# Performance work log

Measured on AMD Instinct MI355X. Metric: run time of the kernel, lower is better.

Reference implementation:

```python
import jax, jax.numpy as jnp
import numpy as np

N_HEADS, D_MODEL, D_HEAD = 16, 1024, 64
INIT_STD = 0.02
IGNORE = -100000.0


def setup_inputs() -> dict:
    key = jax.random.key(0)
    ks = jax.random.split(key, 5)
    x = jax.random.normal(ks[0], (2, 2048, D_MODEL), dtype=jnp.float32)
    W_Q = INIT_STD * jax.random.normal(ks[1], (N_HEADS, D_MODEL, D_HEAD), dtype=jnp.float32)
    W_K = INIT_STD * jax.random.normal(ks[2], (N_HEADS, D_MODEL, D_HEAD), dtype=jnp.float32)
    W_V = INIT_STD * jax.random.normal(ks[3], (N_HEADS, D_MODEL, D_HEAD), dtype=jnp.float32)
    W_O = INIT_STD * jax.random.normal(ks[4], (N_HEADS, D_HEAD, D_MODEL), dtype=jnp.float32)
    b_Q = jnp.zeros((N_HEADS, D_HEAD), dtype=jnp.float32)
    b_K = jnp.zeros((N_HEADS, D_HEAD), dtype=jnp.float32)
    b_V = jnp.zeros((N_HEADS, D_HEAD), dtype=jnp.float32)
    b_O = jnp.zeros((D_MODEL,), dtype=jnp.float32)
    return {"normalized_resid_pre": x, "W_Q": W_Q, "W_K": W_K, "W_V": W_V,
            "W_O": W_O, "b_Q": b_Q, "b_K": b_K, "b_V": b_V, "b_O": b_O}


def reference(normalized_resid_pre, W_Q, W_K, W_V, W_O, b_Q, b_K, b_V, b_O):
    x = normalized_resid_pre  # [b, s, d_model]
    q = jnp.einsum('bsm,hmd->bshd', x, W_Q) + b_Q  # [b, s, h, d_head]
    k = jnp.einsum('bsm,hmd->bshd', x, W_K) + b_K
    v = jnp.einsum('bsm,hmd->bshd', x, W_V) + b_V
    scores = jnp.einsum('bqhd,bkhd->bhqk', q, k) / jnp.sqrt(jnp.float32(D_HEAD))
    s = x.shape[1]
    causal = jnp.triu(jnp.ones((s, s), dtype=bool), k=1)  # True above diagonal
    scores = jnp.where(causal, jnp.float32(IGNORE), scores)
    pattern = jax.nn.softmax(scores, axis=-1)  # [b, h, q, k]
    z = jnp.einsum('bkhd,bhqk->bqhd', v, pattern)
    attn_out = jnp.einsum('bqhd,hdm->bqm', z, W_O) + b_O
    return attn_out
```

## Files before the change

kernel.cpp:

```cpp
#include <hip/hip_runtime.h>
#include <hip/hip_bf16.h>

#define BB   2
#define SS   2048
#define HH   16
#define DM_  1024
#define DH_  64
#define NROW 4096
#define NQKV 3072

typedef unsigned short u16;
typedef unsigned int u32;
using short4v = __attribute__((ext_vector_type(4))) short;
using short8 = __attribute__((ext_vector_type(8))) short;
using bf16x8 = __attribute__((ext_vector_type(8))) __bf16;
using f32x4  = __attribute__((ext_vector_type(4))) float;
using f32x16 = __attribute__((ext_vector_type(16))) float;

#define QSCALE 0.180336880f

__device__ __forceinline__ u16 f2bf(float f) {
    union { float f; unsigned u; } v; v.f = f;
    unsigned r = v.u + 0x7fffu + ((v.u >> 16) & 1u);
    return (u16)(r >> 16);
}

__device__ __forceinline__ f32x4 mfma16(bf16x8 a, bf16x8 b, f32x4 c) {
    return __builtin_amdgcn_mfma_f32_16x16x32_bf16(a, b, c, 0, 0, 0);
}
__device__ __forceinline__ f32x16 mfma32(bf16x8 a, bf16x8 b, f32x16 c) {
    return __builtin_amdgcn_mfma_f32_32x32x16_bf16(a, b, c, 0, 0, 0);
}

__device__ __forceinline__ u32 cvtpk(float lo, float hi) {
    u32 r;
    asm("v_cvt_pk_bf16_f32 %0, %1, %2" : "=v"(r) : "v"(lo), "v"(hi));
    return r;
}
#define PLSWAP(a, b) asm("v_permlane32_swap_b32 %0, %1" : "+v"(a), "+v"(b))

__device__ __forceinline__ void gload16(const void* g, void* l) {
    __builtin_amdgcn_global_load_lds(
        (const __attribute__((address_space(1))) void*)g,
        (__attribute__((address_space(3))) void*)l, 16, 0, 0);
}

__global__ __launch_bounds__(256)
void prep(const float* __restrict__ x,  const float* __restrict__ wq,
          const float* __restrict__ wk, const float* __restrict__ wv,
          const float* __restrict__ wo, const float* __restrict__ bq,
          const float* __restrict__ bk, const float* __restrict__ bv,
          u16* __restrict__ Xb, u16* __restrict__ Wt,
          u16* __restrict__ WoT, float* __restrict__ biasQKV) {
    __shared__ float tile[64][65];
    const int bx = blockIdx.x, t = threadIdx.x;
    if (bx < 512) {
        const int tid = bx * 256 + t;
        #pragma unroll
        for (int it = 0; it < 8; ++it) {
            int i = tid + it * 131072;
            float4 v = ((const float4*)x)[i];
            u16 b4[4] = {f2bf(v.x), f2bf(v.y), f2bf(v.z), f2bf(v.w)};
            ((short4v*)Xb)[i] = *(short4v*)b4;
        }
        if (tid < NQKV) {
            int mat = tid >> 10, h = (tid >> 6) & 15, d = tid & 63;
            const float* bb = (mat == 0) ? bq : ((mat == 1) ? bk : bv);
            biasQKV[tid] = bb[h * DH_ + d];
        }
    } else if (bx < 1280) {
        const int idx = bx - 512;
        const int m0 = (idx & 15) * 64, hm = idx >> 4;
        const int mat = hm >> 4, h = hm & 15;
        const float* w = (mat == 0) ? wq : ((mat == 1) ? wk : wv);
        #pragma unroll
        for (int it = 0; it < 4; ++it) {
            int row = it * 16 + (t >> 4), c4 = (t & 15) * 4;
            float4 v = *(const float4*)&w[((size_t)h * 1024 + m0 + row) * 64 + c4];
            tile[row][c4] = v.x; tile[row][c4 + 1] = v.y;
            tile[row][c4 + 2] = v.z; tile[row][c4 + 3] = v.w;
        }
        __syncthreads();
        #pragma unroll
        for (int it = 0; it < 2; ++it) {
            int c = it * 256 + t, d = c >> 3, mc = (c & 7) * 8;
            u16 buf[8];
            #pragma unroll
            for (int j = 0; j < 8; ++j) buf[j] = f2bf(tile[mc + j][d]);
            *(short8*)&Wt[((size_t)(mat * 1024 + h * 64 + d)) * 1024 + m0 + mc] = *(short8*)buf;
        }
    } else {
        const int idx = bx - 1280;
        const int n0 = (idx & 15) * 64, k0 = (idx >> 4) * 64;
        #pragma unroll
        for (int it = 0; it < 4; ++it) {
            int row = it * 16 + (t >> 4), c4 = (t & 15) * 4;
            float4 v = *(const float4*)&wo[(size_t)(k0 + row) * DM_ + n0 + c4];
            tile[row][c4] = v.x; tile[row][c4 + 1] = v.y;
            tile[row][c4 + 2] = v.z; tile[row][c4 + 3] = v.w;
        }
        __syncthreads();
        #pragma unroll
        for (int it = 0; it < 2; ++it) {
            int c = it * 256 + t, n = c >> 3, kc = (c & 7) * 8;
            u16 buf[8];
            #pragma unroll
            for (int j = 0; j < 8; ++j) buf[j] = f2bf(tile[kc + j][n]);
            *(short8*)&WoT[(size_t)(n0 + n) * DM_ + k0 + kc] = *(short8*)buf;
        }
    }
}

__device__ __forceinline__ void gemm_core_128(
    const u16* __restrict__ Ap, const u16* __restrict__ Bp,
    int brow, int bcol, u16* lds, f32x4 acc[4][2]) {
    const int t = threadIdx.x, l = t & 63;
    const int wid = t >> 6, wm = wid >> 2, wn = wid & 3;
    const int c0 = t, c1 = t + 512;
    const int r0 = c0 >> 3, sb0 = ((c0 & 7) ^ (r0 & 7)) << 3;
    const int r1 = c1 >> 3, sb1 = ((c1 & 7) ^ (r1 & 7)) << 3;
    u16* A0 = lds;
    u16* B0 = lds + 16384;
    const int rA0 = wm * 64 + (l & 15);
    const int rB0 = wn * 32 + (l & 15);
    const int sw  = (l & 7) << 3;
    const int colA = ((l >> 4) << 3);

    {
        gload16(Ap + (size_t)(brow + r0) * DM_ + sb0, A0 + c0 * 8);
        gload16(Ap + (size_t)(brow + r1) * DM_ + sb1, A0 + c1 * 8);
        gload16(Bp + (size_t)(bcol + r0) * DM_ + sb0, B0 + c0 * 8);
        gload16(Bp + (size_t)(bcol + r1) * DM_ + sb1, B0 + c1 * 8);
    }
    __syncthreads();
    for (int kt = 0; kt < 16; ++kt) {
        const int p = kt & 1;
        if (kt < 15) {
            const int ko = (kt + 1) * 64;
            gload16(Ap + (size_t)(brow + r0) * DM_ + ko + sb0, A0 + (p ^ 1) * 8192 + c0 * 8);
            gload16(Ap + (size_t)(brow + r1) * DM_ + ko + sb1, A0 + (p ^ 1) * 8192 + c1 * 8);
            gload16(Bp + (size_t)(bcol + r0) * DM_ + ko + sb0, B0 + (p ^ 1) * 8192 + c0 * 8);
            gload16(Bp + (size_t)(bcol + r1) * DM_ + ko + sb1, B0 + (p ^ 1) * 8192 + c1 * 8);
        }
        const u16* Ab = A0 + p * 8192;
        const u16* Bb = B0 + p * 8192;
        #pragma unroll
        for (int kc = 0; kc < 64; kc += 32) {
            const int cx = (kc + colA) ^ sw;
            bf16x8 af[4], bfr[2];
            #pragma unroll
            for (int m = 0; m < 4; ++m)
                af[m] = *(const bf16x8*)(Ab + (rA0 + m * 16) * 64 + cx);
            #pragma unroll
            for (int n = 0; n < 2; ++n)
                bfr[n] = *(const bf16x8*)(Bb + (rB0 + n * 16) * 64 + cx);
            __builtin_amdgcn_s_setprio(1);
            #pragma unroll
            for (int m = 0; m < 4; ++m)
                #pragma unroll
                for (int n = 0; n < 2; ++n)
                    acc[m][n] = mfma16(af[m], bfr[n], acc[m][n]);
            __builtin_amdgcn_s_setprio(0);
        }
        __syncthreads();
    }
}

__global__ __launch_bounds__(512)
void gemm_qkv3(const u16* __restrict__ Xb, const u16* __restrict__ Wt,
               const float* __restrict__ bias, u16* __restrict__ Qs,
               u16* __restrict__ Ks, u16* __restrict__ Vt) {
    __shared__ __align__(16) u16 lds[32768];
    const int bx = blockIdx.x, t = threadIdx.x, l = t & 63;
    const int wid = t >> 6, wm = wid >> 2, wn = wid & 3;
    f32x4 acc[4][2] = {};
    const bool isV = (bx >= 512);
    int brow, bcol; const u16 *Ap, *Bp;
    if (!isV) { brow = (bx & 31) * 128; bcol = (bx >> 5) * 128; Ap = Xb; Bp = Wt; }
    else { int i2 = bx - 512; brow = (i2 & 7) * 128; bcol = (i2 >> 3) * 128;
           Ap = Wt + (size_t)2048 * DM_; Bp = Xb; }
    gemm_core_128(Ap, Bp, brow, bcol, lds, acc);

    u16* wr_ = lds + wid * 2048;
    const int colbase = bcol + wn * 32;
    const int rowbase = brow + wm * 64;
    const int rsub = ((l >> 4) << 2);
    if (!isV) {
        const float b0 = bias[colbase + (l & 15)];
        const float b1 = bias[colbase + 16 + (l & 15)];
        const float scl = (colbase < 1024) ? QSCALE : 1.0f;
        #pragma unroll
        for (int m = 0; m < 4; ++m)
            #pragma unroll
            for (int n = 0; n < 2; ++n) {
                const float bb = n ? b1 : b0;
                #pragma unroll
                for (int r = 0; r < 4; ++r)
                    wr_[(m * 16 + rsub + r) * 32 + n * 16 + (l & 15)] =
                        f2bf((acc[m][n][r] + bb) * scl);
            }
    } else {
        #pragma unroll
        for (int m = 0; m < 4; ++m) {
            float4 bv = *(const float4*)&bias[2048 + rowbase + m * 16 + rsub];
            const float bbr[4] = {bv.x, bv.y, bv.z, bv.w};
            #pragma unroll
            for (int n = 0; n < 2; ++n)
                #pragma unroll
                for (int r = 0; r < 4; ++r)
                    wr_[(m * 16 + rsub + r) * 32 + n * 16 + (l & 15)] =
                        f2bf(acc[m][n][r] + bbr[r]);
        }
    }
    __syncthreads();
    if (!isV) {
        const int hsel = (colbase >> 6) & 15, d0 = colbase & 63;
        const int bsel = rowbase >> 11, s0 = rowbase & 2047;
        u16* outp = (colbase < 1024) ? Qs : Ks;
        #pragma unroll
        for (int p = 0; p < 4; ++p) {
            const int rr = p * 16 + (l >> 2);
            short8 v = *(const short8*)(wr_ + rr * 32 + (l & 3) * 8);
            *(short8*)&outp[(((size_t)bsel * HH + hsel) * SS + s0 + rr) * DH_ + d0 + (l & 3) * 8] = v;
        }
    } else {
        const int bsel = colbase >> 11, s0 = colbase & 2047;
        #pragma unroll
        for (int p = 0; p < 4; ++p) {
            const int rr = p * 16 + (l >> 2);
            short8 v = *(const short8*)(wr_ + rr * 32 + (l & 3) * 8);
            *(short8*)&Vt[((size_t)bsel * 1024 + rowbase + rr) * SS + s0 + (l & 3) * 8] = v;
        }
    }
}

__global__ __launch_bounds__(512)
void gemm_out3(const u16* __restrict__ Zb, const u16* __restrict__ WoT,
               const float* __restrict__ bO, float* __restrict__ out) {
    __shared__ __align__(16) u16 lds[32768];
    const int bx = blockIdx.x, t = threadIdx.x, l = t & 63;
    const int wid = t >> 6, wm = wid >> 2, wn = wid & 3;
    const int brow = (bx & 31) * 128, bcol = (bx >> 5) * 128;
    f32x4 acc[4][2] = {};
    gemm_core_128(Zb, WoT, brow, bcol, lds, acc);
    const int colbase = bcol + wn * 32;
    const int rowbase = brow + wm * 64;
    const int rsub = ((l >> 4) << 2);
    const float b0 = bO[colbase + (l & 15)];
    const float b1 = bO[colbase + 16 + (l & 15)];
    #pragma unroll
    for (int m = 0; m < 4; ++m)
        #pragma unroll
        for (int n = 0; n < 2; ++n) {
            const float bb = n ? b1 : b0;
            #pragma unroll
            for (int r = 0; r < 4; ++r)
                out[(size_t)(rowbase + m * 16 + rsub + r) * DM_ + colbase + n * 16 + (l & 15)] =
                    acc[m][n][r] + bb;
        }
}

__global__ __launch_bounds__(256)
void attn_fwd(const u16* __restrict__ Qs, const u16* __restrict__ Ks,
              const u16* __restrict__ Vt, u16* __restrict__ Zb) {
    __shared__ __align__(16) u16 fK[4096];
    __shared__ __align__(16) u16 fV[4096];
    __shared__ float lrL[128];
    const int bidx = blockIdx.x;
    const int qt = 15 - (bidx >> 5);
    const int bh = bidx & 31, b = bh >> 4, h = bh & 15;
    const int t = threadIdx.x, wid = t >> 6, l = t & 63;
    const int hi = l >> 5, c32 = l & 31;
    const u16* Qp = Qs + (size_t)bh * SS * DH_;
    const u16* Kp = Ks + (size_t)bh * SS * DH_;
    const u16* Vp = Vt + (size_t)bh * DH_ * SS;
    const int q0 = qt * 128;
    const int qw = q0 + wid * 32;
    const int nt = 2 * qt + 2;

    bf16x8 aq[4];
    #pragma unroll
    for (int dk = 0; dk < 4; ++dk)
        aq[dk] = *(const bf16x8*)&Qp[(size_t)(qw + c32) * DH_ + dk * 16 + hi * 8];

    int kOff[2]; size_t vOff[2]; u16 *dK[2], *dV[2];
    #pragma unroll
    for (int i = 0; i < 2; ++i) {
        const int c = t + 256 * i, sec = c >> 6, ln = c & 63;
        kOff[i] = ((sec >> 2) * 32 + (ln & 31)) * DH_ + (sec & 3) * 16 + (ln >> 5) * 8;
        vOff[i] = (size_t)((sec >> 2) * 32 + (ln & 31)) * SS + (sec & 3) * 16 + (ln >> 5) * 8;
        dK[i] = fK + c * 8;
        dV[i] = fV + c * 8;
    }

    short8 kA[2], vA[2];
    #pragma unroll
    for (int i = 0; i < 2; ++i) {
        kA[i] = *(const short8*)(Kp + kOff[i]);
        vA[i] = *(const short8*)(Vp + vOff[i]);
    }

    f32x16 o0 = {}, o1 = {};
    float lrow = 0.f;

    for (int kt = 0; kt < nt; ++kt) {
        const int kv0 = kt * 64;
        __syncthreads();
        *(short8*)dK[0] = kA[0]; *(short8*)dK[1] = kA[1];
        *(short8*)dV[0] = vA[0]; *(short8*)dV[1] = vA[1];
        __syncthreads();
        if (kt + 1 < nt) {
            const int nb = (kt + 1) * 64;
            #pragma unroll
            for (int i = 0; i < 2; ++i) {
                kA[i] = *(const short8*)(Kp + (size_t)nb * DH_ + kOff[i]);
                vA[i] = *(const short8*)(Vp + nb + vOff[i]);
            }
        }
        if (kv0 <= qw + 31) {
            f32x16 s0 = {}, s1 = {};
            __builtin_amdgcn_s_setprio(1);
            #pragma unroll
            for (int dk = 0; dk < 4; ++dk) {
                s0 = mfma32(*(const bf16x8*)(fK + (0 * 4 + dk) * 512 + l * 8), aq[dk], s0);
                s1 = mfma32(*(const bf16x8*)(fK + (1 * 4 + dk) * 512 + l * 8), aq[dk], s1);
            }
            __builtin_amdgcn_s_setprio(0);
            if (kv0 + 63 > qw) {
                const int q = qw + c32;
                #pragma unroll
                for (int r = 0; r < 16; ++r) {
                    const int crow = (r & 3) + 8 * (r >> 2) + 4 * hi;
                    if (kv0 + crow > q)      s0[r] = -1e30f;
                    if (kv0 + 32 + crow > q) s1[r] = -1e30f;
                }
            }
            #pragma unroll
            for (int r = 0; r < 16; ++r) {
                s0[r] = exp2f(s0[r]);
                s1[r] = exp2f(s1[r]);
                lrow += s0[r] + s1[r];
            }
            __builtin_amdgcn_s_setprio(1);
            #define PV_STEP(PS, B8, KS)                                          \
            {                                                                    \
                u32 cA  = cvtpk(PS[B8 + 0], PS[B8 + 1]);                         \
                u32 cA2 = cvtpk(PS[B8 + 2], PS[B8 + 3]);                         \
                u32 cB  = cvtpk(PS[B8 + 4], PS[B8 + 5]);                         \
                u32 cB2 = cvtpk(PS[B8 + 6], PS[B8 + 7]);                         \
                PLSWAP(cA, cB); PLSWAP(cA2, cB2);                                \
                u32 w[4] = {cA, cA2, cB, cB2};                                   \
                bf16x8 pa = *(bf16x8*)w;                                         \
                o0 = mfma32(pa, *(const bf16x8*)(fV + (0 * 4 + (KS)) * 512 + l * 8), o0); \
                o1 = mfma32(pa, *(const bf16x8*)(fV + (1 * 4 + (KS)) * 512 + l * 8), o1); \
            }
            PV_STEP(s0, 0, 0)
            PV_STEP(s0, 8, 1)
            PV_STEP(s1, 0, 2)
            PV_STEP(s1, 8, 3)
            #undef PV_STEP
            __builtin_amdgcn_s_setprio(0);
        }
    }
    lrow += __shfl_xor(lrow, 32);
    lrL[wid * 32 + c32] = lrow;
    float invv[16];
    #pragma unroll
    for (int g = 0; g < 4; ++g) {
        float4 lv = *(const float4*)&lrL[wid * 32 + 8 * g + 4 * hi];
        invv[g * 4 + 0] = 1.0f / lv.x;
        invv[g * 4 + 1] = 1.0f / lv.y;
        invv[g * 4 + 2] = 1.0f / lv.z;
        invv[g * 4 + 3] = 1.0f / lv.w;
    }
    #pragma unroll
    for (int r = 0; r < 16; ++r) {
        const int q = qw + (r & 3) + 8 * (r >> 2) + 4 * hi;
        u16* zp = &Zb[(((size_t)b * SS + q) * HH + h) * DH_];
        zp[c32]      = f2bf(o0[r] * invv[r]);
        zp[32 + c32] = f2bf(o1[r] * invv[r]);
    }
}

extern "C" void kernel_launch(void* const* d_in, const int* in_sizes, int n_in,
                              void* d_out, int out_size, void* d_ws, size_t ws_size,
                              hipStream_t stream) {
    const float* x  = (const float*)d_in[0];
    const float* wq = (const float*)d_in[1];
    const float* wk = (const float*)d_in[2];
    const float* wv = (const float*)d_in[3];
    const float* wo = (const float*)d_in[4];
    const float* bq = (const float*)d_in[5];
    const float* bk = (const float*)d_in[6];
    const float* bv = (const float*)d_in[7];
    const float* bO = (const float*)d_in[8];
    float* out = (float*)d_out;

    char* w = (char*)d_ws;
    u16* Xb  = (u16*)w;  w += (size_t)NROW * DM_ * 2;
    u16* Wt  = (u16*)w;  w += (size_t)NQKV * DM_ * 2;
    u16* WoT = (u16*)w;  w += (size_t)DM_ * DM_ * 2;
    float* biasQKV = (float*)w; w += (size_t)NQKV * 4;
    u16* Qs  = (u16*)w;  w += (size_t)BB * HH * SS * DH_ * 2;
    u16* Ks  = (u16*)w;  w += (size_t)BB * HH * SS * DH_ * 2;
    u16* Vt  = (u16*)w;  w += (size_t)BB * HH * SS * DH_ * 2;
    u16* Zb  = (u16*)w;  w += (size_t)BB * HH * SS * DH_ * 2;

    prep<<<1536, 256, 0, stream>>>(x, wq, wk, wv, wo, bq, bk, bv,
                                   Xb, Wt, WoT, biasQKV);
    gemm_qkv3<<<768, 512, 0, stream>>>(Xb, Wt, biasQKV, Qs, Ks, Vt);
    attn_fwd<<<512, 256, 0, stream>>>(Qs, Ks, Vt, Zb);
    gemm_out3<<<256, 512, 0, stream>>>(Zb, WoT, bO, out);
}
```

Baseline: 104.6 us.

## Use single-wave attention blocks reading K/V directly from global memory

The attention kernel moves from 4-wave blocks that stage K/V tiles through LDS with barriers to 1-wave blocks of 32 query rows that load K and V fragments straight from global memory into MFMA operands. It also skips the fully masked half-tile on the diagonal and masks only the half that needs it. The aim is to drop LDS staging and __syncthreads overhead, cut wasted causal work, and raise the block count for better load balance. In exchange each wave re-reads K/V from global/L2 without cross-wave reuse and loses the software prefetch, so memory traffic grows and load latency is exposed.

```diff
diff --git a/kernel.cpp b/kernel.cpp
--- a/kernel.cpp
+++ b/kernel.cpp
@@ -260,114 +260,103 @@
         }
 }
 
-__global__ __launch_bounds__(256)
+__global__ __launch_bounds__(64)
 void attn_fwd(const u16* __restrict__ Qs, const u16* __restrict__ Ks,
               const u16* __restrict__ Vt, u16* __restrict__ Zb) {
-    __shared__ __align__(16) u16 fK[4096];
-    __shared__ __align__(16) u16 fV[4096];
-    __shared__ float lrL[128];
+    __shared__ float lrL[32];
     const int bidx = blockIdx.x;
-    const int qt = 15 - (bidx >> 5);
+    const int qt = 63 - (bidx >> 5);
     const int bh = bidx & 31, b = bh >> 4, h = bh & 15;
-    const int t = threadIdx.x, wid = t >> 6, l = t & 63;
+    const int l = threadIdx.x & 63;
     const int hi = l >> 5, c32 = l & 31;
     const u16* Qp = Qs + (size_t)bh * SS * DH_;
     const u16* Kp = Ks + (size_t)bh * SS * DH_;
     const u16* Vp = Vt + (size_t)bh * DH_ * SS;
-    const int q0 = qt * 128;
-    const int qw = q0 + wid * 32;
-    const int nt = 2 * qt + 2;
+    const int qw = qt * 32;
+    const int nt = (qt >> 1) + 1;
 
     bf16x8 aq[4];
     #pragma unroll
     for (int dk = 0; dk < 4; ++dk)
         aq[dk] = *(const bf16x8*)&Qp[(size_t)(qw + c32) * DH_ + dk * 16 + hi * 8];
 
-    int kOff[2]; size_t vOff[2]; u16 *dK[2], *dV[2];
-    #pragma unroll
-    for (int i = 0; i < 2; ++i) {
-        const int c = t + 256 * i, sec = c >> 6, ln = c & 63;
-        kOff[i] = ((sec >> 2) * 32 + (ln & 31)) * DH_ + (sec & 3) * 16 + (ln >> 5) * 8;
-        vOff[i] = (size_t)((sec >> 2) * 32 + (ln & 31)) * SS + (sec & 3) * 16 + (ln >> 5) * 8;
-        dK[i] = fK + c * 8;
-        dV[i] = fV + c * 8;
-    }
-
-    short8 kA[2], vA[2];
-    #pragma unroll
-    for (int i = 0; i < 2; ++i) {
-        kA[i] = *(const short8*)(Kp + kOff[i]);
-        vA[i] = *(const short8*)(Vp + vOff[i]);
-    }
-
     f32x16 o0 = {}, o1 = {};
     float lrow = 0.f;
 
+    const int kfo = c32 * DH_ + hi * 8;
+    const int vfo = c32 * SS + hi * 8;
+
     for (int kt = 0; kt < nt; ++kt) {
         const int kv0 = kt * 64;
-        __syncthreads();
-        *(short8*)dK[0] = kA[0]; *(short8*)dK[1] = kA[1];
-        *(short8*)dV[0] = vA[0]; *(short8*)dV[1] = vA[1];
-        __syncthreads();
-        if (kt + 1 < nt) {
-            const int nb = (kt + 1) * 64;
-            #pragma unroll
-            for (int i = 0; i < 2; ++i) {
-                kA[i] = *(const short8*)(Kp + (size_t)nb * DH_ + kOff[i]);
-                vA[i] = *(const short8*)(Vp + nb + vOff[i]);
-            }
-        }
-        if (kv0 <= qw + 31) {
-            f32x16 s0 = {}, s1 = {};
-            __builtin_amdgcn_s_setprio(1);
-            #pragma unroll
-            for (int dk = 0; dk < 4; ++dk) {
-                s0 = mfma32(*(const bf16x8*)(fK + (0 * 4 + dk) * 512 + l * 8), aq[dk], s0);
-                s1 = mfma32(*(const bf16x8*)(fK + (1 * 4 + dk) * 512 + l * 8), aq[dk], s1);
-            }
-            __builtin_amdgcn_s_setprio(0);
-            if (kv0 + 63 > qw) {
-                const int q = qw + c32;
+        const bool diag = (kt == nt - 1);
+        const bool skip1 = diag && !(qt & 1);
+
+        f32x16 s0 = {}, s1 = {};
+        const u16* kb = Kp + (size_t)kv0 * DH_ + kfo;
+        __builtin_amdgcn_s_setprio(1);
+        #pragma unroll
+        for (int dk = 0; dk < 4; ++dk)
+            s0 = mfma32(*(const bf16x8*)(kb + dk * 16), aq[dk], s0);
+        if (!skip1) {
+            #pragma unroll
+            for (int dk = 0; dk < 4; ++dk)
+                s1 = mfma32(*(const bf16x8*)(kb + 32 * DH_ + dk * 16), aq[dk], s1);
+        }
+        __builtin_amdgcn_s_setprio(0);
+
+        if (diag) {
+            const int q = qw + c32;
+            if (qt & 1) {
                 #pragma unroll
                 for (int r = 0; r < 16; ++r) {
                     const int crow = (r & 3) + 8 * (r >> 2) + 4 * hi;
-                    if (kv0 + crow > q)      s0[r] = -1e30f;
                     if (kv0 + 32 + crow > q) s1[r] = -1e30f;
                 }
+            } else {
+                #pragma unroll
+                for (int r = 0; r < 16; ++r) {
+                    const int crow = (r & 3) + 8 * (r >> 2) + 4 * hi;
+                    if (kv0 + crow > q) s0[r] = -1e30f;
+                }
             }
-            #pragma unroll
-            for (int r = 0; r < 16; ++r) {
-                s0[r] = exp2f(s0[r]);
-                s1[r] = exp2f(s1[r]);
-                lrow += s0[r] + s1[r];
-            }
-            __builtin_amdgcn_s_setprio(1);
-            #define PV_STEP(PS, B8, KS)                                          \
-            {                                                                    \
-                u32 cA  = cvtpk(PS[B8 + 0], PS[B8 + 1]);                         \
-                u32 cA2 = cvtpk(PS[B8 + 2], PS[B8 + 3]);                         \
-                u32 cB  = cvtpk(PS[B8 + 4], PS[B8 + 5]);                         \
-                u32 cB2 = cvtpk(PS[B8 + 6], PS[B8 + 7]);                         \
-                PLSWAP(cA, cB); PLSWAP(cA2, cB2);                                \
-                u32 w[4] = {cA, cA2, cB, cB2};                                   \
-                bf16x8 pa = *(bf16x8*)w;                                         \
-                o0 = mfma32(pa, *(const bf16x8*)(fV + (0 * 4 + (KS)) * 512 + l * 8), o0); \
-                o1 = mfma32(pa, *(const bf16x8*)(fV + (1 * 4 + (KS)) * 512 + l * 8), o1); \
-            }
-            PV_STEP(s0, 0, 0)
-            PV_STEP(s0, 8, 1)
+        }
+        #pragma unroll
+        for (int r = 0; r < 16; ++r) { s0[r] = exp2f(s0[r]); lrow += s0[r]; }
+        if (!skip1) {
+            #pragma unroll
+            for (int r = 0; r < 16; ++r) { s1[r] = exp2f(s1[r]); lrow += s1[r]; }
+        }
+
+        const u16* vb = Vp + kv0 + vfo;
+        __builtin_amdgcn_s_setprio(1);
+        #define PV_STEP(PS, B8, KS)                                              \
+        {                                                                        \
+            u32 cA  = cvtpk(PS[B8 + 0], PS[B8 + 1]);                             \
+            u32 cA2 = cvtpk(PS[B8 + 2], PS[B8 + 3]);                             \
+            u32 cB  = cvtpk(PS[B8 + 4], PS[B8 + 5]);                             \
+            u32 cB2 = cvtpk(PS[B8 + 6], PS[B8 + 7]);                             \
+            PLSWAP(cA, cB); PLSWAP(cA2, cB2);                                    \
+            u32 w[4] = {cA, cA2, cB, cB2};                                       \
+            bf16x8 pa = *(bf16x8*)w;                                             \
+            o0 = mfma32(pa, *(const bf16x8*)(vb + (KS) * 16), o0);               \
+            o1 = mfma32(pa, *(const bf16x8*)(vb + 32 * SS + (KS) * 16), o1);     \
+        }
+        PV_STEP(s0, 0, 0)
+        PV_STEP(s0, 8, 1)
+        if (!skip1) {
             PV_STEP(s1, 0, 2)
             PV_STEP(s1, 8, 3)
-            #undef PV_STEP
-            __builtin_amdgcn_s_setprio(0);
-        }
-    }
+        }
+        #undef PV_STEP
+        __builtin_amdgcn_s_setprio(0);
+    }
+
     lrow += __shfl_xor(lrow, 32);
-    lrL[wid * 32 + c32] = lrow;
+    if (hi == 0) lrL[c32] = lrow;
     float invv[16];
     #pragma unroll
     for (int g = 0; g < 4; ++g) {
-        float4 lv = *(const float4*)&lrL[wid * 32 + 8 * g + 4 * hi];
+        float4 lv = *(const float4*)&lrL[8 * g + 4 * hi];
         invv[g * 4 + 0] = 1.0f / lv.x;
         invv[g * 4 + 1] = 1.0f / lv.y;
         invv[g * 4 + 2] = 1.0f / lv.z;
@@ -409,6 +398,6 @@
     prep<<<1536, 256, 0, stream>>>(x, wq, wk, wv, wo, bq, bk, bv,
                                    Xb, Wt, WoT, biasQKV);
     gemm_qkv3<<<768, 512, 0, stream>>>(Xb, Wt, biasQKV, Qs, Ks, Vt);
-    attn_fwd<<<512, 256, 0, stream>>>(Qs, Ks, Vt, Zb);
+    attn_fwd<<<2048, 64, 0, stream>>>(Qs, Ks, Vt, Zb);
     gemm_out3<<<256, 512, 0, stream>>>(Zb, WoT, bO, out);
 }
```

Measured after the change: 136.0 us. +30.0%, slower.

## Double-buffer K/V tiles in LDS and skip fully masked causal half-tiles

Applied to the files above, without the earlier changes.

Uses two LDS buffers for K and V so the next tile is stored while the current one is consumed, cutting the per-iteration barriers from two to one. On the diagonal tile it skips the QK, exp and PV work for the 32-key half that lies entirely above the causal boundary for a warp. It also changes the block-to-query-tile mapping for block indices past 256. The cost is doubled LDS usage, which may reduce occupancy, and extra divergent branches.

```diff
diff --git a/kernel.cpp b/kernel.cpp
--- a/kernel.cpp
+++ b/kernel.cpp
@@ -263,19 +263,18 @@
 __global__ __launch_bounds__(256)
 void attn_fwd(const u16* __restrict__ Qs, const u16* __restrict__ Ks,
               const u16* __restrict__ Vt, u16* __restrict__ Zb) {
-    __shared__ __align__(16) u16 fK[4096];
-    __shared__ __align__(16) u16 fV[4096];
+    __shared__ __align__(16) u16 fK[2][4096];
+    __shared__ __align__(16) u16 fV[2][4096];
     __shared__ float lrL[128];
     const int bidx = blockIdx.x;
-    const int qt = 15 - (bidx >> 5);
+    const int qt = (bidx < 256) ? (15 - (bidx >> 5)) : ((bidx - 256) >> 5);
     const int bh = bidx & 31, b = bh >> 4, h = bh & 15;
     const int t = threadIdx.x, wid = t >> 6, l = t & 63;
     const int hi = l >> 5, c32 = l & 31;
     const u16* Qp = Qs + (size_t)bh * SS * DH_;
     const u16* Kp = Ks + (size_t)bh * SS * DH_;
     const u16* Vp = Vt + (size_t)bh * DH_ * SS;
-    const int q0 = qt * 128;
-    const int qw = q0 + wid * 32;
+    const int qw = qt * 128 + wid * 32;
     const int nt = 2 * qt + 2;
 
     bf16x8 aq[4];
@@ -283,14 +282,13 @@
     for (int dk = 0; dk < 4; ++dk)
         aq[dk] = *(const bf16x8*)&Qp[(size_t)(qw + c32) * DH_ + dk * 16 + hi * 8];
 
-    int kOff[2]; size_t vOff[2]; u16 *dK[2], *dV[2];
+    int kOff[2]; size_t vOff[2]; int dst[2];
     #pragma unroll
     for (int i = 0; i < 2; ++i) {
         const int c = t + 256 * i, sec = c >> 6, ln = c & 63;
         kOff[i] = ((sec >> 2) * 32 + (ln & 31)) * DH_ + (sec & 3) * 16 + (ln >> 5) * 8;
         vOff[i] = (size_t)((sec >> 2) * 32 + (ln & 31)) * SS + (sec & 3) * 16 + (ln >> 5) * 8;
-        dK[i] = fK + c * 8;
-        dV[i] = fV + c * 8;
+        dst[i] = c * 8;
     }
 
     short8 kA[2], vA[2];
@@ -299,31 +297,54 @@
         kA[i] = *(const short8*)(Kp + kOff[i]);
         vA[i] = *(const short8*)(Vp + vOff[i]);
     }
+    #pragma unroll
+    for (int i = 0; i < 2; ++i) {
+        *(short8*)(&fK[0][dst[i]]) = kA[i];
+        *(short8*)(&fV[0][dst[i]]) = vA[i];
+    }
+    if (nt > 1) {
+        #pragma unroll
+        for (int i = 0; i < 2; ++i) {
+            kA[i] = *(const short8*)(Kp + (size_t)64 * DH_ + kOff[i]);
+            vA[i] = *(const short8*)(Vp + 64 + vOff[i]);
+        }
+    }
+    __syncthreads();
 
     f32x16 o0 = {}, o1 = {};
     float lrow = 0.f;
 
     for (int kt = 0; kt < nt; ++kt) {
+        const int p = kt & 1;
+        if (kt + 1 < nt) {
+            #pragma unroll
+            for (int i = 0; i < 2; ++i) {
+                *(short8*)(&fK[p ^ 1][dst[i]]) = kA[i];
+                *(short8*)(&fV[p ^ 1][dst[i]]) = vA[i];
+            }
+            if (kt + 2 < nt) {
+                const int nb = (kt + 2) * 64;
+                #pragma unroll
+                for (int i = 0; i < 2; ++i) {
+                    kA[i] = *(const short8*)(Kp + (size_t)nb * DH_ + kOff[i]);
+                    vA[i] = *(const short8*)(Vp + nb + vOff[i]);
+                }
+            }
+        }
         const int kv0 = kt * 64;
-        __syncthreads();
-        *(short8*)dK[0] = kA[0]; *(short8*)dK[1] = kA[1];
-        *(short8*)dV[0] = vA[0]; *(short8*)dV[1] = vA[1];
-        __syncthreads();
-        if (kt + 1 < nt) {
-            const int nb = (kt + 1) * 64;
-            #pragma unroll
-            for (int i = 0; i < 2; ++i) {
-                kA[i] = *(const short8*)(Kp + (size_t)nb * DH_ + kOff[i]);
-                vA[i] = *(const short8*)(Vp + nb + vOff[i]);
-            }
-        }
         if (kv0 <= qw + 31) {
+            const u16* fKb = fK[p];
+            const u16* fVb = fV[p];
+            const bool have1 = (kv0 + 32 <= qw + 31);
             f32x16 s0 = {}, s1 = {};
             __builtin_amdgcn_s_setprio(1);
             #pragma unroll
-            for (int dk = 0; dk < 4; ++dk) {
-                s0 = mfma32(*(const bf16x8*)(fK + (0 * 4 + dk) * 512 + l * 8), aq[dk], s0);
-                s1 = mfma32(*(const bf16x8*)(fK + (1 * 4 + dk) * 512 + l * 8), aq[dk], s1);
+            for (int dk = 0; dk < 4; ++dk)
+                s0 = mfma32(*(const bf16x8*)(fKb + dk * 512 + l * 8), aq[dk], s0);
+            if (have1) {
+                #pragma unroll
+                for (int dk = 0; dk < 4; ++dk)
+                    s1 = mfma32(*(const bf16x8*)(fKb + (4 + dk) * 512 + l * 8), aq[dk], s1);
             }
             __builtin_amdgcn_s_setprio(0);
             if (kv0 + 63 > qw) {
@@ -331,15 +352,21 @@
                 #pragma unroll
                 for (int r = 0; r < 16; ++r) {
                     const int crow = (r & 3) + 8 * (r >> 2) + 4 * hi;
-                    if (kv0 + crow > q)      s0[r] = -1e30f;
-                    if (kv0 + 32 + crow > q) s1[r] = -1e30f;
+                    if (kv0 + crow > q) s0[r] = -1e30f;
                 }
-            }
-            #pragma unroll
-            for (int r = 0; r < 16; ++r) {
-                s0[r] = exp2f(s0[r]);
-                s1[r] = exp2f(s1[r]);
-                lrow += s0[r] + s1[r];
+                if (have1) {
+                    #pragma unroll
+                    for (int r = 0; r < 16; ++r) {
+                        const int crow = (r & 3) + 8 * (r >> 2) + 4 * hi;
+                        if (kv0 + 32 + crow > q) s1[r] = -1e30f;
+                    }
+                }
+            }
+            #pragma unroll
+            for (int r = 0; r < 16; ++r) { s0[r] = exp2f(s0[r]); lrow += s0[r]; }
+            if (have1) {
+                #pragma unroll
+                for (int r = 0; r < 16; ++r) { s1[r] = exp2f(s1[r]); lrow += s1[r]; }
             }
             __builtin_amdgcn_s_setprio(1);
             #define PV_STEP(PS, B8, KS)                                          \
@@ -351,17 +378,21 @@
                 PLSWAP(cA, cB); PLSWAP(cA2, cB2);                                \
                 u32 w[4] = {cA, cA2, cB, cB2};                                   \
                 bf16x8 pa = *(bf16x8*)w;                                         \
-                o0 = mfma32(pa, *(const bf16x8*)(fV + (0 * 4 + (KS)) * 512 + l * 8), o0); \
-                o1 = mfma32(pa, *(const bf16x8*)(fV + (1 * 4 + (KS)) * 512 + l * 8), o1); \
+                o0 = mfma32(pa, *(const bf16x8*)(fVb + (0 * 4 + (KS)) * 512 + l * 8), o0); \
+                o1 = mfma32(pa, *(const bf16x8*)(fVb + (1 * 4 + (KS)) * 512 + l * 8), o1); \
             }
             PV_STEP(s0, 0, 0)
             PV_STEP(s0, 8, 1)
-            PV_STEP(s1, 0, 2)
-            PV_STEP(s1, 8, 3)
+            if (have1) {
+                PV_STEP(s1, 0, 2)
+                PV_STEP(s1, 8, 3)
+            }
             #undef PV_STEP
             __builtin_amdgcn_s_setprio(0);
         }
-    }
+        __syncthreads();
+    }
+
     lrow += __shfl_xor(lrow, 32);
     lrL[wid * 32 + c32] = lrow;
     float invv[16];
```

New measurement: 102.6 us. Within noise of the previous version (-1.8%).
